# Kernel optimization log

Hardware: AMD Instinct MI355X
Metric: run time of the kernel (lower is better)

## Reference

```python
import jax, jax.numpy as jnp
import numpy as np

B, S, D, U = 32, 2048, 1024, 1024


def setup_inputs() -> dict:
    key = jax.random.key(0)
    ks = jax.random.split(key, 10)
    s = 0.02
    return {
        "dec_hidden": jax.random.normal(ks[0], (B, D), jnp.float32),
        "enc_output": jax.random.normal(ks[1], (B, S, D), jnp.float32),
        "enc_pad_mask": jnp.ones((B, S), jnp.int32),  # accepted but unused, as in the original
        "use_coverage": True,
        "prev_coverage": jax.random.uniform(ks[2], (B, S, 1), jnp.float32),
        "Ws_w": jax.random.normal(ks[3], (D, U), jnp.float32) * s,
        "Ws_b": jnp.zeros((U,), jnp.float32),
        "Wh_w": jax.random.normal(ks[4], (D, U), jnp.float32) * s,
        "Wh_b": jnp.zeros((U,), jnp.float32),
        "Wc_w": jax.random.normal(ks[5], (1, U), jnp.float32) * s,
        "Wc_b": jnp.zeros((U,), jnp.float32),
        "V_w": jax.random.normal(ks[6], (U, 1), jnp.float32) * s,
        "V_b": jnp.zeros((1,), jnp.float32),
    }


def reference(dec_hidden, enc_output, enc_pad_mask, use_coverage, prev_coverage,
              Ws_w, Ws_b, Wh_w, Wh_b, Wc_w, Wc_b, V_w, V_b):
    # W_h(dec_hidden) with time axis: [B, 1, U]
    h = (dec_hidden @ Wh_w + Wh_b)[:, None, :]
    # W_s(enc_output): [B, S, U]
    feat = jnp.einsum('bsd,du->bsu', enc_output, Ws_w) + Ws_b + h
    if use_coverage and prev_coverage is not None:
        # W_c(prev_coverage): [B, S, 1] @ [1, U] -> [B, S, U]
        feat = feat + prev_coverage @ Wc_w + Wc_b
        score = jnp.tanh(feat) @ V_w + V_b            # [B, S, 1]
        attention_weights = jax.nn.softmax(score, axis=1)
        coverage = attention_weights + prev_coverage
    else:
        score = jnp.tanh(feat) @ V_w + V_b
        attention_weights = jax.nn.softmax(score, axis=1)
        coverage = attention_weights if use_coverage else []
    # weighted sum over sequence axis: [B, D]
    context_vector = jnp.sum(attention_weights * enc_output, axis=1)
    return context_vector, jnp.squeeze(attention_weights, -1), coverage
```

## Files before the change

### kernel.cpp

```cpp
#include <hip/hip_runtime.h>
#include <hip/hip_bf16.h>

namespace {

constexpr int kB = 32;
constexpr int kS = 2048;
constexpr int kD = 1024;
constexpr int kU = 1024;

constexpr int BM = 256;
constexpr int BN = 256;
constexpr int BK = 64;
constexpr int kKT = kD / BK;
constexpr int kMT = (kB * kS) / BM;
constexpr int kNT = kU / BN;
constexpr size_t kHalf = 16384;
constexpr size_t kTileChunk = 2 * kHalf;
constexpr size_t kPanel = (size_t)kKT * kTileChunk;

typedef __attribute__((ext_vector_type(8))) short bf16x8;
typedef __attribute__((ext_vector_type(4))) float f32x4;

__device__ __forceinline__ unsigned short f2bf(float x) {
  union { __hip_bfloat16 h; unsigned short u; } c;
  c.h = __float2bfloat16(x);
  return c.u;
}

__device__ __forceinline__ float bf2f(unsigned short u) {
  union { unsigned int i; float f; } c;
  c.i = ((unsigned int)u) << 16;
  return c.f;
}

__device__ __forceinline__ float tanh_fast(float x) {
  float e = __expf(2.0f * x);
  return 1.0f - 2.0f * __builtin_amdgcn_rcpf(e + 1.0f);
}

__device__ __forceinline__ void gload16(const void* g, void* l) {
  __builtin_amdgcn_global_load_lds(
      (const __attribute__((address_space(1))) void*)g,
      (__attribute__((address_space(3))) void*)l, 16, 0, 0);
}


__global__ __launch_bounds__(256) void h2b_kernel(
    const float* __restrict__ dec, const float* __restrict__ Whw,
    const float* __restrict__ Whb, const float* __restrict__ Wsb,
    const float* __restrict__ Wcb, float* __restrict__ h2) {
  const int u = blockIdx.x * 64 + (threadIdx.x & 63);
  const int b = blockIdx.y * 4 + (threadIdx.x >> 6);
  float acc = 0.f;
  const float* dh = dec + b * kD;
  #pragma unroll 8
  for (int d = 0; d < kD; ++d) acc += dh[d] * Whw[(size_t)d * kU + u];
  h2[b * kU + u] = acc + Whb[u] + Wsb[u] + Wcb[u];
}


__global__ __launch_bounds__(256) void convA_kernel(
    const float* __restrict__ enc, unsigned char* __restrict__ encT) {
  const size_t e = ((size_t)blockIdx.x * 256 + threadIdx.x) * 8;
  const int r = (int)(e >> 10), d0 = (int)(e & 1023);
  float4 v0 = *(const float4*)(enc + e);
  float4 v1 = *(const float4*)(enc + e + 4);
  uint4 p;
  p.x = (unsigned)f2bf(v0.x) | ((unsigned)f2bf(v0.y) << 16);
  p.y = (unsigned)f2bf(v0.z) | ((unsigned)f2bf(v0.w) << 16);
  p.z = (unsigned)f2bf(v1.x) | ((unsigned)f2bf(v1.y) << 16);
  p.w = (unsigned)f2bf(v1.z) | ((unsigned)f2bf(v1.w) << 16);
  const int mt = r >> 8, rh = (r >> 7) & 1, row = r & 127;
  const int kt = d0 >> 6, c8 = (d0 & 63) >> 3;
  unsigned char* dst = encT + (size_t)mt * kPanel + (size_t)kt * kTileChunk +
                       (size_t)rh * kHalf + row * 128 +
                       (((unsigned)c8 << 4) ^ (((unsigned)row & 7) << 4));
  *(uint4*)dst = p;
}

__global__ __launch_bounds__(256) void tpose2_kernel(
    const float* __restrict__ W, unsigned char* __restrict__ Bt) {
  __shared__ float tile[32][33];
  const int u0 = blockIdx.x * 32, d0 = blockIdx.y * 32;
  const int tx = threadIdx.x, ty = threadIdx.y;
  #pragma unroll
  for (int i = 0; i < 4; ++i)
    tile[ty + i * 8][tx] = W[(size_t)(d0 + ty + i * 8) * kU + u0 + tx];
  __syncthreads();
  #pragma unroll
  for (int i = 0; i < 4; ++i) {
    const int u = u0 + ty + i * 8, d = d0 + tx;
    const int nt = u >> 8, gh = (u >> 7) & 1, n = u & 127;
    const int kt = d >> 6, c = d & 63;
    *(unsigned short*)(Bt + (size_t)nt * kPanel + (size_t)kt * kTileChunk +
                       (size_t)gh * kHalf + n * 128 +
                       (((((unsigned)c >> 3) << 4) ^ (((unsigned)n & 7) << 4)) +
                        (c & 7) * 2)) = f2bf(tile[tx][ty + i * 8]);
  }
}

#define MFMA_BF16(a, b, c) __builtin_amdgcn_mfma_f32_16x16x32_bf16((a), (b), (c), 0, 0, 0)

#define READ_A8(AF, ABASE, QR)                                                 \
  _Pragma("unroll")                                                            \
  for (int rfl = 0; rfl < 4; ++rfl) {                                          \
    _Pragma("unroll")                                                          \
    for (int ks = 0; ks < 2; ++ks) {                                           \
      const int row_ = ((QR)*4 + rfl) * 16 + lr;                               \
      AF[rfl][ks] = *(const bf16x8*)((ABASE) + row_ * 128 +                    \
                                     ((ks * 64 + lq * 16) ^ ((lr & 7) << 4))); \
    }                                                                          \
  }

#define READ_B4(BF, BBASE, QC)                                                 \
  _Pragma("unroll")                                                            \
  for (int cfl = 0; cfl < 2; ++cfl) {                                          \
    _Pragma("unroll")                                                          \
    for (int ks = 0; ks < 2; ++ks) {                                           \
      const int row_ = ((QC)*2 + cfl) * 16 + lr;                               \
      BF[cfl][ks] = *(const bf16x8*)((BBASE) + row_ * 128 +                    \
                                     ((ks * 64 + lq * 16) ^ ((lr & 7) << 4))); \
    }                                                                          \
  }

#define MF16(QR, QC, AF, BF)                                                   \
  _Pragma("unroll")                                                            \
  for (int ks = 0; ks < 2; ++ks) {                                             \
    _Pragma("unroll")                                                          \
    for (int rfl = 0; rfl < 4; ++rfl) {                                        \
      _Pragma("unroll")                                                        \
      for (int cfl = 0; cfl < 2; ++cfl)                                        \
        acc[(QR)*4 + rfl][(QC)*2 + cfl] =                                      \
            MFMA_BF16(AF[rfl][ks], BF[cfl][ks], acc[(QR)*4 + rfl][(QC)*2 + cfl]); \
    }                                                                          \
  }

#define STAGE2(GSRC, LDST)                                                     \
  gload16((GSRC) + so0, (LDST) + so0);                                         \
  gload16((GSRC) + so1, (LDST) + so1);

#define FENCE asm volatile("" ::: "memory")
#define BARRIER { FENCE; __builtin_amdgcn_s_barrier(); FENCE; }

__global__ __launch_bounds__(512, 1) void score_gemm4_kernel(
    const unsigned char* __restrict__ encT, const unsigned char* __restrict__ Bt,
    const float* __restrict__ h2, const float* __restrict__ pc,
    const float* __restrict__ Wcw, const float* __restrict__ Vw,
    float* __restrict__ scorep) {
  __shared__ __attribute__((aligned(16))) unsigned char lds[131072];

  const int tid = threadIdx.x;
  const int lane = tid & 63;
  const int w = tid >> 6;
  const int lr = lane & 15, lq = lane >> 4;
  const int wm = w >> 2;
  const int wn = w & 3;
  const int g = wn >> 1;

  const int work = (blockIdx.x & 7) * 128 + (blockIdx.x >> 3);
  const int mtile = work >> 2, ntile = work & 3;

  const unsigned char* Ab = encT + (size_t)mtile * kPanel;
  const unsigned char* Bb = Bt + (size_t)ntile * kPanel;
  const int so0 = tid * 16;
  const int so1 = tid * 16 + 8192;

  unsigned char* Ad0 = lds + (size_t)wm * kHalf;
  unsigned char* Ad1 = lds + (2 + wm) * kHalf;
  unsigned char* Bd0 = lds + 65536 + (size_t)g * kHalf + (wn & 1) * 8192;
  unsigned char* Bd1 = lds + 65536 + (2 + g) * kHalf + (wn & 1) * 8192;
  unsigned char* aSlot[2][2] = {{lds, lds + kHalf}, {lds + 2 * kHalf, lds + 3 * kHalf}};
  unsigned char* bSlot[2][2] = {{lds + 65536, lds + 65536 + kHalf},
                                {lds + 65536 + 2 * kHalf, lds + 65536 + 3 * kHalf}};

  f32x4 acc[8][4];
  #pragma unroll
  for (int i = 0; i < 8; ++i)
    #pragma unroll
    for (int j = 0; j < 4; ++j) acc[i][j] = (f32x4){0.f, 0.f, 0.f, 0.f};

  bf16x8 af[4][2], b0[2][2], b1[2][2];

  STAGE2(Bb, bSlot[0][0]);
  STAGE2(Bb + kHalf, bSlot[0][1]);
  STAGE2(Ab, aSlot[0][0]);
  STAGE2(Ab + kHalf, aSlot[0][1]);
  STAGE2(Bb + kTileChunk, bSlot[1][0]);
  STAGE2(Bb + kTileChunk + kHalf, bSlot[1][1]);
  asm volatile("s_waitcnt vmcnt(4)" ::: "memory");
  BARRIER;

  for (int i = 0; i < kKT / 2; ++i) {
    const int t2 = (i < kKT / 2 - 1) ? 2 * i + 2 : 2 * i;
    const int t3 = (i < kKT / 2 - 1) ? 2 * i + 3 : 2 * i;
    const unsigned char* sA1 = Ab + (size_t)(2 * i + 1) * kTileChunk;
    const unsigned char* sA2 = Ab + (size_t)t2 * kTileChunk;
    const unsigned char* sB2 = Bb + (size_t)t2 * kTileChunk;
    const unsigned char* sB3 = Bb + (size_t)t3 * kTileChunk;

    READ_A8(af, Ad0, 0);
    READ_B4(b0, Bd0, 0);
    STAGE2(sA1, aSlot[1][0]);
    BARRIER;
    __builtin_amdgcn_s_setprio(1);
    MF16(0, 0, af, b0);
    __builtin_amdgcn_s_setprio(0);
    BARRIER;

    READ_B4(b1, Bd0, 1);
    STAGE2(sA1 + kHalf, aSlot[1][1]);
    BARRIER;
    __builtin_amdgcn_s_setprio(1);
    MF16(0, 1, af, b1);
    __builtin_amdgcn_s_setprio(0);
    BARRIER;

    READ_A8(af, Ad0, 1);
    STAGE2(sB2, bSlot[0][0]);
    BARRIER;
    __builtin_amdgcn_s_setprio(1);
    MF16(1, 0, af, b0);
    __builtin_amdgcn_s_setprio(0);
    BARRIER;

    STAGE2(sB2 + kHalf, bSlot[0][1]);
    asm volatile("s_waitcnt vmcnt(4)" ::: "memory");
    BARRIER;
    __builtin_amdgcn_s_setprio(1);
    MF16(1, 1, af, b1);
    __builtin_amdgcn_s_setprio(0);
    BARRIER;

    READ_A8(af, Ad1, 0);
    READ_B4(b0, Bd1, 0);
    STAGE2(sA2, aSlot[0][0]);
    BARRIER;
    __builtin_amdgcn_s_setprio(1);
    MF16(0, 0, af, b0);
    __builtin_amdgcn_s_setprio(0);
    BARRIER;

    READ_B4(b1, Bd1, 1);
    STAGE2(sA2 + kHalf, aSlot[0][1]);
    BARRIER;
    __builtin_amdgcn_s_setprio(1);
    MF16(0, 1, af, b1);
    __builtin_amdgcn_s_setprio(0);
    BARRIER;

    READ_A8(af, Ad1, 1);
    STAGE2(sB3, bSlot[1][0]);
    BARRIER;
    __builtin_amdgcn_s_setprio(1);
    MF16(1, 0, af, b0);
    __builtin_amdgcn_s_setprio(0);
    BARRIER;

    STAGE2(sB3 + kHalf, bSlot[1][1]);
    asm volatile("s_waitcnt vmcnt(4)" ::: "memory");
    BARRIER;
    __builtin_amdgcn_s_setprio(1);
    MF16(1, 1, af, b1);
    __builtin_amdgcn_s_setprio(0);
    BARRIER;
  }
  asm volatile("s_waitcnt vmcnt(0)" ::: "memory");

  const int bidx = mtile >> 3;
  float hv[4], wv[4], vv[4];
  #pragma unroll
  for (int cf = 0; cf < 4; ++cf) {
    const int u = ntile * BN + wn * 64 + cf * 16 + lr;
    hv[cf] = h2[bidx * kU + u];
    wv[cf] = Wcw[u];
    vv[cf] = Vw[u];
  }
  float* plane = scorep + (size_t)(ntile * 4 + wn) * (kB * kS);
  #pragma unroll
  for (int rf = 0; rf < 8; ++rf) {
    #pragma unroll
    for (int j = 0; j < 4; ++j) {
      const int r = mtile * BM + wm * 128 + rf * 16 + lq * 4 + j;
      const float pcv = pc[r];
      float partial = 0.f;
      #pragma unroll
      for (int cf = 0; cf < 4; ++cf) {
        const float feat = acc[rf][cf][j] + hv[cf] + pcv * wv[cf];
        partial += tanh_fast(feat) * vv[cf];
      }
      partial += __shfl_xor(partial, 1);
      partial += __shfl_xor(partial, 2);
      partial += __shfl_xor(partial, 4);
      partial += __shfl_xor(partial, 8);
      if (lr == 0) plane[r] = partial;
    }
  }
}

__global__ __launch_bounds__(256) void softmax2_kernel(
    const float* __restrict__ scorep, const float* __restrict__ pc,
    float* __restrict__ attn, float* __restrict__ cov) {
  const int b = blockIdx.x, tid = threadIdx.x;
  const int lane = tid & 63, wid = tid >> 6;
  const size_t base = (size_t)b * kS + tid * 8;
  float v[8] = {0.f, 0.f, 0.f, 0.f, 0.f, 0.f, 0.f, 0.f};
  #pragma unroll
  for (int p = 0; p < 16; ++p) {
    const float* s = scorep + (size_t)p * (kB * kS) + base;
    float4 a = *(const float4*)(s);
    float4 c = *(const float4*)(s + 4);
    v[0] += a.x; v[1] += a.y; v[2] += a.z; v[3] += a.w;
    v[4] += c.x; v[5] += c.y; v[6] += c.z; v[7] += c.w;
  }
  float m = v[0];
  #pragma unroll
  for (int i = 1; i < 8; ++i) m = fmaxf(m, v[i]);
  #pragma unroll
  for (int msk = 1; msk < 64; msk <<= 1) m = fmaxf(m, __shfl_xor(m, msk));
  __shared__ float redm[4], reds[4];
  if (lane == 0) redm[wid] = m;
  __syncthreads();
  m = fmaxf(fmaxf(redm[0], redm[1]), fmaxf(redm[2], redm[3]));
  float e[8], sum = 0.f;
  #pragma unroll
  for (int i = 0; i < 8; ++i) { e[i] = __expf(v[i] - m); sum += e[i]; }
  #pragma unroll
  for (int msk = 1; msk < 64; msk <<= 1) sum += __shfl_xor(sum, msk);
  if (lane == 0) reds[wid] = sum;
  __syncthreads();
  sum = reds[0] + reds[1] + reds[2] + reds[3];
  const float inv = 1.0f / sum;
  float pv[8], a[8], c[8];
  const float* p = pc + base;
  *(float4*)(pv) = *(const float4*)(p);
  *(float4*)(pv + 4) = *(const float4*)(p + 4);
  #pragma unroll
  for (int i = 0; i < 8; ++i) { a[i] = e[i] * inv; c[i] = a[i] + pv[i]; }
  *(float4*)(attn + base) = *(float4*)(a);
  *(float4*)(attn + base + 4) = *(float4*)(a + 4);
  *(float4*)(cov + base) = *(float4*)(c);
  *(float4*)(cov + base + 4) = *(float4*)(c + 4);
}

__global__ __launch_bounds__(256) void context2_kernel(
    const unsigned char* __restrict__ encT, const float* __restrict__ attn,
    float* __restrict__ ctx) {
  const int kt = blockIdx.x;
  const int b = blockIdx.y;
  const int cg = threadIdx.x & 7;
  const int rgrp = threadIdx.x >> 3;
  float acc8[8];
  #pragma unroll
  for (int j = 0; j < 8; ++j) acc8[j] = 0.f;
  const float* ab = attn + (size_t)b * kS;
  for (int it = 0; it < kS / 32; ++it) {
    const int s = it * 32 + rgrp;
    const int r = b * kS + s;
    const int mt = r >> 8, rh = (r >> 7) & 1, row = r & 127;
    const unsigned char* chunk = encT + (size_t)mt * kPanel +
                                 (size_t)kt * kTileChunk + (size_t)rh * kHalf;
    uint4 v = *(const uint4*)(chunk + row * 128 +
                              ((((unsigned)cg << 4) ^ (((unsigned)row & 7) << 4))));
    const float a = ab[s];
    const unsigned int* vw = (const unsigned int*)&v;
    #pragma unroll
    for (int q = 0; q < 4; ++q) {
      acc8[2 * q]     += a * bf2f((unsigned short)(vw[q] & 0xffff));
      acc8[2 * q + 1] += a * bf2f((unsigned short)(vw[q] >> 16));
    }
  }
  __shared__ float red[256 * 8];
  #pragma unroll
  for (int j = 0; j < 8; ++j) red[threadIdx.x * 8 + j] = acc8[j];
  __syncthreads();
  for (int stride = 16; stride > 0; stride >>= 1) {
    if (rgrp < stride) {
      #pragma unroll
      for (int j = 0; j < 8; ++j)
        red[(rgrp * 8 + cg) * 8 + j] += red[((rgrp + stride) * 8 + cg) * 8 + j];
    }
    __syncthreads();
  }
  if (rgrp == 0) {
    #pragma unroll
    for (int j = 0; j < 8; ++j)
      ctx[(size_t)b * kD + kt * 64 + cg * 8 + j] = red[cg * 8 + j];
  }
}


__global__ __launch_bounds__(256) void tpose_fb_kernel(
    const float* __restrict__ W, unsigned short* __restrict__ out) {
  __shared__ float tile[32][33];
  const int u0 = blockIdx.x * 32, d0 = blockIdx.y * 32;
  const int tx = threadIdx.x, ty = threadIdx.y;
  #pragma unroll
  for (int i = 0; i < 4; ++i)
    tile[ty + i * 8][tx] = W[(size_t)(d0 + ty + i * 8) * kU + u0 + tx];
  __syncthreads();
  #pragma unroll
  for (int i = 0; i < 4; ++i)
    out[(size_t)(u0 + ty + i * 8) * kD + d0 + tx] = f2bf(tile[tx][ty + i * 8]);
}

__global__ __launch_bounds__(256, 2) void score_gemm_fb_kernel(
    const float* __restrict__ enc, const unsigned short* __restrict__ WsT,
    const float* __restrict__ h2, const float* __restrict__ pc,
    const float* __restrict__ Wcw, const float* __restrict__ Vw,
    float* __restrict__ score) {
  __shared__ __attribute__((aligned(16))) unsigned char smA[128 * 64 * 2];
  __shared__ __attribute__((aligned(16))) unsigned char smB[128 * 64 * 2];
  const int tid = threadIdx.x;
  const int lane = tid & 63;
  const int wid = tid >> 6;
  const int wr = wid >> 1, wc = wid & 1;
  const int mtile = blockIdx.x >> 3, ntile = blockIdx.x & 7;
  const int r0 = mtile * 128, n0 = ntile * 128;
  f32x4 acc[4][4];
  #pragma unroll
  for (int i = 0; i < 4; ++i)
    #pragma unroll
    for (int j = 0; j < 4; ++j) acc[i][j] = (f32x4){0.f, 0.f, 0.f, 0.f};
  const int kqA = tid & 15;
  const int rowA = tid >> 4;
  const int kcB = tid & 7;
  const int nB = tid >> 3;
  float4 aReg[8];
  uint4 bReg[4];
  #pragma unroll
  for (int i = 0; i < 8; ++i)
    aReg[i] = *(const float4*)(enc + (size_t)(r0 + rowA + 16 * i) * kD + kqA * 4);
  #pragma unroll
  for (int i = 0; i < 4; ++i)
    bReg[i] = *(const uint4*)(WsT + (size_t)(n0 + nB + 32 * i) * kD + kcB * 8);
  const int lr = lane & 15, lq = lane >> 4;
  for (int k0 = 0; k0 < kD; k0 += 64) {
    #pragma unroll
    for (int i = 0; i < 8; ++i) {
      const int row = rowA + 16 * i;
      uint2 p;
      p.x = (unsigned)f2bf(aReg[i].x) | ((unsigned)f2bf(aReg[i].y) << 16);
      p.y = (unsigned)f2bf(aReg[i].z) | ((unsigned)f2bf(aReg[i].w) << 16);
      *(uint2*)(smA + row * 128 + ((kqA * 8) ^ ((row & 7) << 4))) = p;
    }
    #pragma unroll
    for (int i = 0; i < 4; ++i) {
      const int n = nB + 32 * i;
      *(uint4*)(smB + n * 128 + ((kcB * 16) ^ ((n & 7) << 4))) = bReg[i];
    }
    __syncthreads();
    if (k0 + 64 < kD) {
      const int kn = k0 + 64;
      #pragma unroll
      for (int i = 0; i < 8; ++i)
        aReg[i] = *(const float4*)(enc + (size_t)(r0 + rowA + 16 * i) * kD + kn + kqA * 4);
      #pragma unroll
      for (int i = 0; i < 4; ++i)
        bReg[i] = *(const uint4*)(WsT + (size_t)(n0 + nB + 32 * i) * kD + kn + kcB * 8);
    }
    #pragma unroll
    for (int ks = 0; ks < 2; ++ks) {
      const int kb = ks * 64 + lq * 16;
      bf16x8 af2[4], bfr[4];
      #pragma unroll
      for (int fm = 0; fm < 4; ++fm) {
        const int row = wr * 64 + fm * 16 + lr;
        af2[fm] = *(const bf16x8*)(smA + row * 128 + (kb ^ ((row & 7) << 4)));
      }
      #pragma unroll
      for (int fn = 0; fn < 4; ++fn) {
        const int n = wc * 64 + fn * 16 + lr;
        bfr[fn] = *(const bf16x8*)(smB + n * 128 + (kb ^ ((n & 7) << 4)));
      }
      #pragma unroll
      for (int fm = 0; fm < 4; ++fm)
        #pragma unroll
        for (int fn = 0; fn < 4; ++fn)
          acc[fm][fn] = MFMA_BF16(af2[fm], bfr[fn], acc[fm][fn]);
    }
    __syncthreads();
  }
  const int bidx = r0 >> 11;
  float hv[4], wv[4], vv[4];
  #pragma unroll
  for (int fn = 0; fn < 4; ++fn) {
    const int u = n0 + wc * 64 + fn * 16 + lr;
    hv[fn] = h2[bidx * kU + u];
    wv[fn] = Wcw[u];
    vv[fn] = Vw[u];
  }
  #pragma unroll
  for (int fm = 0; fm < 4; ++fm) {
    #pragma unroll
    for (int j = 0; j < 4; ++j) {
      const int r = r0 + wr * 64 + fm * 16 + lq * 4 + j;
      const float pcv = pc[r];
      float partial = 0.f;
      #pragma unroll
      for (int fn = 0; fn < 4; ++fn) {
        const float feat = acc[fm][fn][j] + hv[fn] + pcv * wv[fn];
        partial += tanh_fast(feat) * vv[fn];
      }
      partial += __shfl_xor(partial, 1);
      partial += __shfl_xor(partial, 2);
      partial += __shfl_xor(partial, 4);
      partial += __shfl_xor(partial, 8);
      if (lr == 0) atomicAdd(&score[r], partial);
    }
  }
}

__global__ __launch_bounds__(256) void softmax_fb_kernel(
    const float* __restrict__ score, const float* __restrict__ pc,
    float* __restrict__ attn, float* __restrict__ cov) {
  const int b = blockIdx.x, tid = threadIdx.x;
  const int lane = tid & 63, wid = tid >> 6;
  const float* s = score + (size_t)b * kS;
  float v[8];
  *(float4*)(v) = *(const float4*)(s + tid * 8);
  *(float4*)(v + 4) = *(const float4*)(s + tid * 8 + 4);
  float m = v[0];
  #pragma unroll
  for (int i = 1; i < 8; ++i) m = fmaxf(m, v[i]);
  #pragma unroll
  for (int msk = 1; msk < 64; msk <<= 1) m = fmaxf(m, __shfl_xor(m, msk));
  __shared__ float redm[4], reds[4];
  if (lane == 0) redm[wid] = m;
  __syncthreads();
  m = fmaxf(fmaxf(redm[0], redm[1]), fmaxf(redm[2], redm[3]));
  float e[8], sum = 0.f;
  #pragma unroll
  for (int i = 0; i < 8; ++i) { e[i] = __expf(v[i] - m); sum += e[i]; }
  #pragma unroll
  for (int msk = 1; msk < 64; msk <<= 1) sum += __shfl_xor(sum, msk);
  if (lane == 0) reds[wid] = sum;
  __syncthreads();
  sum = reds[0] + reds[1] + reds[2] + reds[3];
  const float inv = 1.0f / sum;
  float pv[8], a[8], c[8];
  const float* p = pc + (size_t)b * kS + tid * 8;
  *(float4*)(pv) = *(const float4*)(p);
  *(float4*)(pv + 4) = *(const float4*)(p + 4);
  #pragma unroll
  for (int i = 0; i < 8; ++i) { a[i] = e[i] * inv; c[i] = a[i] + pv[i]; }
  *(float4*)(attn + (size_t)b * kS + tid * 8) = *(float4*)(a);
  *(float4*)(attn + (size_t)b * kS + tid * 8 + 4) = *(float4*)(a + 4);
  *(float4*)(cov + (size_t)b * kS + tid * 8) = *(float4*)(c);
  *(float4*)(cov + (size_t)b * kS + tid * 8 + 4) = *(float4*)(c + 4);
}

__global__ __launch_bounds__(256) void context_fb_kernel(
    const float* __restrict__ enc, const float* __restrict__ attn,
    float* __restrict__ ctx) {
  const int b = blockIdx.z;
  const int s0 = blockIdx.y * 256;
  const int d = blockIdx.x * 256 + threadIdx.x;
  const float* e = enc + ((size_t)b * kS + s0) * kD + d;
  const float* a = attn + (size_t)b * kS + s0;
  float acc = 0.f;
  #pragma unroll 8
  for (int s = 0; s < 256; ++s) acc += a[s] * e[(size_t)s * kD];
  atomicAdd(&ctx[b * kD + d], acc);
}

}

extern "C" void kernel_launch(void* const* d_in, const int* in_sizes, int n_in,
                              void* d_out, int out_size, void* d_ws, size_t ws_size,
                              hipStream_t stream) {
  (void)in_sizes; (void)n_in; (void)out_size;
  const float* dec = (const float*)d_in[0];
  const float* enc = (const float*)d_in[1];
  const float* pc  = (const float*)d_in[4];
  const float* Wsw = (const float*)d_in[5];
  const float* Wsb = (const float*)d_in[6];
  const float* Whw = (const float*)d_in[7];
  const float* Whb = (const float*)d_in[8];
  const float* Wcw = (const float*)d_in[9];
  const float* Wcb = (const float*)d_in[10];
  const float* Vw  = (const float*)d_in[11];

  float* ctx  = (float*)d_out;
  float* attn = (float*)d_out + kB * kD;
  float* cov  = attn + kB * kS;

  unsigned char* ws = (unsigned char*)d_ws;

  const size_t encT_sz = (size_t)kB * kS * kD * 2;
  const size_t Bt_sz   = (size_t)kU * kD * 2;
  const size_t h2_sz   = (size_t)kB * kU * 4;
  const size_t sp_sz   = (size_t)16 * kB * kS * 4;
  const size_t need    = encT_sz + Bt_sz + h2_sz + sp_sz;

  if (ws_size >= need) {
    unsigned char* encT = ws;
    unsigned char* Bt   = ws + encT_sz;
    float* h2     = (float*)(ws + encT_sz + Bt_sz);
    float* scorep = (float*)(ws + encT_sz + Bt_sz + h2_sz);

    convA_kernel<<<dim3((kB * kS * kD / 8) / 256), 256, 0, stream>>>(enc, encT);
    tpose2_kernel<<<dim3(kU / 32, kD / 32), dim3(32, 8), 0, stream>>>(Wsw, Bt);
    h2b_kernel<<<dim3(kU / 64, kB / 4), 256, 0, stream>>>(dec, Whw, Whb, Wsb, Wcb, h2);
    score_gemm4_kernel<<<dim3(kMT * kNT), 512, 0, stream>>>(
        encT, Bt, h2, pc, Wcw, Vw, scorep);
    softmax2_kernel<<<dim3(kB), 256, 0, stream>>>(scorep, pc, attn, cov);
    context2_kernel<<<dim3(kD / 64, kB), 256, 0, stream>>>(encT, attn, ctx);
  } else {
    unsigned short* WsT = (unsigned short*)ws;
    float* h2    = (float*)(ws + (size_t)2 * 1024 * 1024);
    float* score = (float*)(ws + (size_t)2 * 1024 * 1024 + 131072);
    hipMemsetAsync(score, 0, kB * kS * sizeof(float), stream);
    hipMemsetAsync(ctx, 0, kB * kD * sizeof(float), stream);
    h2b_kernel<<<dim3(kU / 64, kB / 4), 256, 0, stream>>>(dec, Whw, Whb, Wsb, Wcb, h2);
    tpose_fb_kernel<<<dim3(kU / 32, kD / 32), dim3(32, 8), 0, stream>>>(Wsw, WsT);
    score_gemm_fb_kernel<<<dim3(4096), 256, 0, stream>>>(
        enc, WsT, h2, pc, Wcw, Vw, score);
    softmax_fb_kernel<<<dim3(kB), 256, 0, stream>>>(score, pc, attn, cov);
    context_fb_kernel<<<dim3(kD / 256, kS / 256, kB), 256, 0, stream>>>(enc, attn, ctx);
  }
}
```

Before: 315.8 us.

## Software-pipeline MFMA blocks one phase behind LDS fragment reads in score GEMM

The main GEMM loop now double-buffers the A fragments in registers (a0/a1) and shifts each MFMA block one phase later than its LDS reads. Each phase's math then runs on fragments loaded in an earlier phase while new reads are in flight, instead of waiting on reads issued just before it. The second barrier of each phase now waits on lgkmcnt(0), and the final MF16 block is peeled after the loop. This raises register pressure with a second A fragment set, which risks spills under the 512-thread launch bound.

```diff
diff --git a/kernel.cpp b/kernel.cpp
--- a/kernel.cpp
+++ b/kernel.cpp
@@ -140,9 +140,11 @@
   gload16((GSRC) + so1, (LDST) + so1);
 
 #define FENCE asm volatile("" ::: "memory")
-#define BARRIER { FENCE; __builtin_amdgcn_s_barrier(); FENCE; }
-
-__global__ __launch_bounds__(512, 1) void score_gemm4_kernel(
+#define BAR_A { FENCE; __builtin_amdgcn_s_barrier(); FENCE; }
+#define BAR_B { asm volatile("s_waitcnt lgkmcnt(0)" ::: "memory");             \
+                __builtin_amdgcn_s_barrier(); FENCE; }
+
+__global__ __launch_bounds__(512, 1) void score_gemm5_kernel(
     const unsigned char* __restrict__ encT, const unsigned char* __restrict__ Bt,
     const float* __restrict__ h2, const float* __restrict__ pc,
     const float* __restrict__ Wcw, const float* __restrict__ Vw,
@@ -179,7 +181,7 @@
     #pragma unroll
     for (int j = 0; j < 4; ++j) acc[i][j] = (f32x4){0.f, 0.f, 0.f, 0.f};
 
-  bf16x8 af[4][2], b0[2][2], b1[2][2];
+  bf16x8 a0[4][2], a1[4][2], b0[2][2], b1[2][2];
 
   STAGE2(Bb, bSlot[0][0]);
   STAGE2(Bb + kHalf, bSlot[0][1]);
@@ -188,7 +190,7 @@
   STAGE2(Bb + kTileChunk, bSlot[1][0]);
   STAGE2(Bb + kTileChunk + kHalf, bSlot[1][1]);
   asm volatile("s_waitcnt vmcnt(4)" ::: "memory");
-  BARRIER;
+  BAR_A;
 
   for (int i = 0; i < kKT / 2; ++i) {
     const int t2 = (i < kKT / 2 - 1) ? 2 * i + 2 : 2 * i;
@@ -198,72 +200,75 @@
     const unsigned char* sB2 = Bb + (size_t)t2 * kTileChunk;
     const unsigned char* sB3 = Bb + (size_t)t3 * kTileChunk;
 
-    READ_A8(af, Ad0, 0);
+    READ_A8(a0, Ad0, 0);
     READ_B4(b0, Bd0, 0);
     STAGE2(sA1, aSlot[1][0]);
-    BARRIER;
-    __builtin_amdgcn_s_setprio(1);
-    MF16(0, 0, af, b0);
-    __builtin_amdgcn_s_setprio(0);
-    BARRIER;
+    BAR_A;
+    if (i) {
+      __builtin_amdgcn_s_setprio(1);
+      MF16(1, 1, a1, b1);
+      __builtin_amdgcn_s_setprio(0);
+    }
+    BAR_B;
 
     READ_B4(b1, Bd0, 1);
     STAGE2(sA1 + kHalf, aSlot[1][1]);
-    BARRIER;
+    BAR_A;
     __builtin_amdgcn_s_setprio(1);
-    MF16(0, 1, af, b1);
+    MF16(0, 0, a0, b0);
     __builtin_amdgcn_s_setprio(0);
-    BARRIER;
-
-    READ_A8(af, Ad0, 1);
+    BAR_B;
+
+    READ_A8(a1, Ad0, 1);
     STAGE2(sB2, bSlot[0][0]);
-    BARRIER;
+    BAR_A;
     __builtin_amdgcn_s_setprio(1);
-    MF16(1, 0, af, b0);
+    MF16(0, 1, a0, b1);
     __builtin_amdgcn_s_setprio(0);
-    BARRIER;
+    BAR_B;
 
     STAGE2(sB2 + kHalf, bSlot[0][1]);
     asm volatile("s_waitcnt vmcnt(4)" ::: "memory");
-    BARRIER;
+    BAR_A;
     __builtin_amdgcn_s_setprio(1);
-    MF16(1, 1, af, b1);
+    MF16(1, 0, a1, b0);
     __builtin_amdgcn_s_setprio(0);
-    BARRIER;
-
-    READ_A8(af, Ad1, 0);
+    BAR_B;
+
+    READ_A8(a0, Ad1, 0);
     READ_B4(b0, Bd1, 0);
     STAGE2(sA2, aSlot[0][0]);
-    BARRIER;
+    BAR_A;
     __builtin_amdgcn_s_setprio(1);
-    MF16(0, 0, af, b0);
+    MF16(1, 1, a1, b1);
     __builtin_amdgcn_s_setprio(0);
-    BARRIER;
+    BAR_B;
 
     READ_B4(b1, Bd1, 1);
     STAGE2(sA2 + kHalf, aSlot[0][1]);
-    BARRIER;
+    BAR_A;
     __builtin_amdgcn_s_setprio(1);
-    MF16(0, 1, af, b1);
+    MF16(0, 0, a0, b0);
     __builtin_amdgcn_s_setprio(0);
-    BARRIER;
-
-    READ_A8(af, Ad1, 1);
+    BAR_B;
+
+    READ_A8(a1, Ad1, 1);
     STAGE2(sB3, bSlot[1][0]);
-    BARRIER;
+    BAR_A;
     __builtin_amdgcn_s_setprio(1);
-    MF16(1, 0, af, b0);
+    MF16(0, 1, a0, b1);
     __builtin_amdgcn_s_setprio(0);
-    BARRIER;
+    BAR_B;
 
     STAGE2(sB3 + kHalf, bSlot[1][1]);
     asm volatile("s_waitcnt vmcnt(4)" ::: "memory");
-    BARRIER;
+    BAR_A;
     __builtin_amdgcn_s_setprio(1);
-    MF16(1, 1, af, b1);
+    MF16(1, 0, a1, b0);
     __builtin_amdgcn_s_setprio(0);
-    BARRIER;
-  }
+    BAR_B;
+  }
+  MF16(1, 1, a1, b1);
   asm volatile("s_waitcnt vmcnt(0)" ::: "memory");
 
   const int bidx = mtile >> 3;
@@ -601,7 +606,7 @@
     convA_kernel<<<dim3((kB * kS * kD / 8) / 256), 256, 0, stream>>>(enc, encT);
     tpose2_kernel<<<dim3(kU / 32, kD / 32), dim3(32, 8), 0, stream>>>(Wsw, Bt);
     h2b_kernel<<<dim3(kU / 64, kB / 4), 256, 0, stream>>>(dec, Whw, Whb, Wsb, Wcb, h2);
-    score_gemm4_kernel<<<dim3(kMT * kNT), 512, 0, stream>>>(
+    score_gemm5_kernel<<<dim3(kMT * kNT), 512, 0, stream>>>(
         encT, Bt, h2, pc, Wcw, Vw, scorep);
     softmax2_kernel<<<dim3(kB), 256, 0, stream>>>(scorep, pc, attn, cov);
     context2_kernel<<<dim3(kD / 64, kB), 256, 0, stream>>>(encT, attn, ctx);
```

New measurement: 333.2 us. +5.5%, slower.
